# Performance work log

Measured on AMD Instinct MI355X. Metric: run time of the kernel, lower is better.

Reference implementation:

```python
import jax, jax.numpy as jnp
import numpy as np

# dims matching init_kwargs
B, S, D, DH, E, K = 16, 8192, 256, 512, 8, 2


def setup_inputs() -> dict:
    key = jax.random.key(0)
    k0, k1, k2, k3 = jax.random.split(key, 4)
    scale = 0.02
    x = jax.random.normal(k0, (B, S, D), dtype=jnp.float32)
    gate_w = jax.random.normal(k1, (E, D), dtype=jnp.float32) * scale   # Linear(d_model, E, bias=False): weight [E, D]
    w1 = jax.random.normal(k2, (E, DH, D), dtype=jnp.float32) * scale   # fc1 weight per expert [DH, D]
    b1 = jnp.zeros((E, DH), dtype=jnp.float32)
    w2 = jax.random.normal(k3, (E, D, DH), dtype=jnp.float32) * scale   # fc2 weight per expert [D, DH]
    b2 = jnp.zeros((E, D), dtype=jnp.float32)
    return {"x": x, "gate_w": gate_w, "w1": w1, "b1": b1, "w2": w2, "b2": b2}


def reference(x, gate_w, w1, b1, w2, b2):
    b, s, d = x.shape
    e = gate_w.shape[0]
    xf = x.reshape(-1, d)                      # [T, D]
    T = xf.shape[0]

    # --- TopKRouter ---
    logits = xf @ gate_w.T                     # [T, E]
    probs = jax.nn.softmax(logits, axis=-1)
    topk_p, topk_i = jax.lax.top_k(probs, K)   # [T, K]
    topk_w = topk_p / topk_p.sum(axis=-1, keepdims=True)
    # load-balancing aux loss
    sel_mask = jax.nn.one_hot(topk_i, e, dtype=jnp.float32).sum(axis=1)  # [T, E]
    f_i = sel_mask.mean(axis=0)
    p_i = probs.mean(axis=0)
    aux_loss = e * jnp.sum(f_i * p_i)

    # --- dispatch: dense per-token expert weights (0 for unselected) ---
    dense_w = jnp.zeros((T, e), dtype=x.dtype).at[
        jnp.arange(T)[:, None], topk_i
    ].add(topk_w)                              # [T, E]

    # --- experts: loop over small fixed E; weight is zero for unselected tokens,
    # so this computes the same math as the sparse gather/scatter loop ---
    out = jnp.zeros_like(xf)
    for ei in range(e):
        h = jax.nn.silu(xf @ w1[ei].T + b1[ei])     # [T, DH]
        y = h @ w2[ei].T + b2[ei]                   # [T, D]
        out = out + dense_w[:, ei:ei + 1] * y

    return out.reshape(b, s, d), aux_loss
```

## Files before the change

### kernel.cpp

```cpp
#include <hip/hip_runtime.h>

typedef __attribute__((ext_vector_type(8))) short short8;
typedef __attribute__((ext_vector_type(4))) float f32x4;

#define T_TOK  131072
#define DMODEL 256
#define DHID   512
#define NEXP   8


__device__ __forceinline__ unsigned short f2bf(float f) {
  unsigned int u = __float_as_uint(f);
  u = (u + 0x7FFFu + ((u >> 16) & 1u)) >> 16;
  return (unsigned short)u;
}
__device__ __forceinline__ float bf2f(unsigned short u) {
  return __uint_as_float(((unsigned)u) << 16);
}

__device__ __forceinline__ void gload16(const void* g, void* l) {
  __builtin_amdgcn_global_load_lds(
      (const __attribute__((address_space(1))) void*)g,
      (__attribute__((address_space(3))) void*)l, 16, 0, 0);
}

__global__ void k_wconv(const float* __restrict__ w1, const float* __restrict__ w2,
                        unsigned short* __restrict__ P1, unsigned short* __restrict__ P2) {
  int g = blockIdx.x * 256 + threadIdx.x;
  int e = g >> 14, rem = g & 16383;
  {
    int row = rem >> 5, c = rem & 31;
    int kc = c >> 3, cs = c & 7;
    const float* s = w1 + ((size_t)e * DHID + row) * DMODEL + c * 8;
    short8 v;
#pragma unroll
    for (int j = 0; j < 8; ++j) v[j] = (short)f2bf(s[j]);
    size_t dc = ((size_t)(e * 4 + kc) * 512 + row) * 8 + (cs ^ (row & 7));
    *(short8*)(P1 + dc * 8) = v;
  }
  {
    int row = rem >> 6, c = rem & 63;
    int kc = c >> 3, cs = c & 7;
    const float* s = w2 + ((size_t)e * DMODEL + row) * DHID + c * 8;
    short8 v;
#pragma unroll
    for (int j = 0; j < 8; ++j) v[j] = (short)f2bf(s[j]);
    size_t dc = ((size_t)(e * 8 + kc) * 256 + row) * 8 + (cs ^ (row & 7));
    *(short8*)(P2 + dc * 8) = v;
  }
}

__global__ __launch_bounds__(256) void k_router(
    const float* __restrict__ x, const float* __restrict__ gate,
    unsigned short* __restrict__ xb, int* __restrict__ pack, float2* __restrict__ tkw,
    int* __restrict__ part_cnt, float* __restrict__ part_psum) {
  __shared__ float g[NEXP][DMODEL];
  __shared__ int s_cnt[NEXP];
  __shared__ float s_ps[NEXP];
  int tid = threadIdx.x;
  for (int i = tid; i < NEXP * DMODEL; i += 256) g[i >> 8][i & 255] = gate[i];
  if (tid < NEXP) { s_cnt[tid] = 0; s_ps[tid] = 0.f; }
  __syncthreads();
  int lane = tid & 63, wv = tid >> 6;
  float psacc[NEXP] = {0.f,0.f,0.f,0.f,0.f,0.f,0.f,0.f};
  for (int k = 0; k < 16; ++k) {
    int t = (blockIdx.x << 6) + (wv << 4) + k;
    const float* xr = x + (size_t)t * DMODEL;
    float4 x4 = *(const float4*)(xr + 4 * lane);
    ushort4 u4;
    u4.x = f2bf(x4.x); u4.y = f2bf(x4.y); u4.z = f2bf(x4.z); u4.w = f2bf(x4.w);
    *(ushort4*)(xb + (size_t)t * DMODEL + 4 * lane) = u4;
    double l[NEXP];
#pragma unroll
    for (int e = 0; e < NEXP; ++e) {
      const float4 g4 = *(const float4*)&g[e][4 * lane];
      l[e] = (double)x4.x * (double)g4.x + (double)x4.y * (double)g4.y +
             (double)x4.z * (double)g4.z + (double)x4.w * (double)g4.w;
    }
#pragma unroll
    for (int e = 0; e < NEXP; ++e) {
#pragma unroll
      for (int d = 32; d; d >>= 1) l[e] += __shfl_xor(l[e], d);
    }
    int i1 = 0;
#pragma unroll
    for (int e = 1; e < NEXP; ++e) if (l[e] > l[i1]) i1 = e;
    int i2 = (i1 == 0) ? 1 : 0;
#pragma unroll
    for (int e = 0; e < NEXP; ++e) if (e != i1 && l[e] > l[i2]) i2 = e;
    double m = l[0];
#pragma unroll
    for (int e = 1; e < NEXP; ++e) m = (l[e] > m) ? l[e] : m;
    float pe[NEXP]; float s = 0.f;
#pragma unroll
    for (int e = 0; e < NEXP; ++e) { pe[e] = __expf((float)(l[e] - m)); s += pe[e]; }
    float inv = 1.f / s;
    float p1 = pe[i1] * inv, p2 = pe[i2] * inv;
    float wn = 1.f / (p1 + p2);
    if (lane == 0) {
      pack[t] = i1 | (i2 << 8);
      tkw[t] = make_float2(p1 * wn, p2 * wn);
      atomicAdd(&s_cnt[i1], 1); atomicAdd(&s_cnt[i2], 1);
#pragma unroll
      for (int e = 0; e < NEXP; ++e) psacc[e] += pe[e] * inv;
    }
  }
  if (lane == 0) {
#pragma unroll
    for (int e = 0; e < NEXP; ++e) atomicAdd(&s_ps[e], psacc[e]);
  }
  __syncthreads();
  if (tid < NEXP) {
    part_cnt[blockIdx.x * NEXP + tid] = s_cnt[tid];
    part_psum[blockIdx.x * NEXP + tid] = s_ps[tid];
  }
}

__global__ __launch_bounds__(512) void k_scan(
    const int* __restrict__ part_cnt, const float* __restrict__ part_psum,
    int* __restrict__ block_off, int* __restrict__ cnt_total, float* __restrict__ out) {
  __shared__ float s_ps[NEXP];
  __shared__ int s_ct[NEXP];
  int lane = threadIdx.x & 63, wv = threadIdx.x >> 6;
  int base = lane * 32;
  int lsum = 0; float ps = 0.f;
#pragma unroll 8
  for (int j = 0; j < 32; ++j) {
    lsum += part_cnt[(base + j) * NEXP + wv];
    ps += part_psum[(base + j) * NEXP + wv];
  }
  int incl = lsum;
#pragma unroll
  for (int d = 1; d < 64; d <<= 1) { int t = __shfl_up(incl, d); if (lane >= d) incl += t; }
  int run = incl - lsum;
#pragma unroll 8
  for (int j = 0; j < 32; ++j) {
    int v = part_cnt[(base + j) * NEXP + wv];
    block_off[(base + j) * NEXP + wv] = run;
    run += v;
  }
#pragma unroll
  for (int d = 32; d; d >>= 1) ps += __shfl_xor(ps, d);
  int total = __shfl(incl, 63);
  if (lane == 0) { cnt_total[wv] = total; s_ct[wv] = total; s_ps[wv] = ps; }
  __syncthreads();
  if (threadIdx.x == 0) {
    double aux = 0.0; int rb = 0;
    for (int e = 0; e < NEXP; ++e) {
      aux += ((double)s_ct[e] / 131072.0) * ((double)s_ps[e] / 131072.0);
      cnt_total[8 + e] = rb;
      rb += (s_ct[e] + 255) & ~255;
    }
    out[33554432] = (float)(8.0 * aux);
  }
}

__global__ void k_scatter(const int* __restrict__ pack, float2* tkw,
                          const int* __restrict__ block_off, const int* __restrict__ cnt_total,
                          int* __restrict__ tok_list, float* __restrict__ wt_list) {
  __shared__ int s_loc[NEXP];
  int tid = threadIdx.x;
  if (tid < NEXP) s_loc[tid] = 0;
  __syncthreads();
  int t = (blockIdx.x << 6) + tid;
  int p = pack[t];
  float2 wv = tkw[t];
  int e1 = p & 255, e2 = (p >> 8) & 255;
  int o1 = block_off[blockIdx.x * NEXP + e1];
  int p1 = atomicAdd(&s_loc[e1], 1);
  int i1 = cnt_total[8 + e1] + o1 + p1;
  tok_list[i1] = t; wt_list[i1] = wv.x;
  int o2 = block_off[blockIdx.x * NEXP + e2];
  int p2 = atomicAdd(&s_loc[e2], 1);
  int i2 = cnt_total[8 + e2] + o2 + p2;
  tok_list[i2] = t; wt_list[i2] = wv.y;
  tkw[t] = make_float2(__int_as_float(i1), __int_as_float(i2));
}

__global__ __launch_bounds__(512, 2) void k_gemm1(
    const unsigned short* __restrict__ xb, const unsigned short* __restrict__ P1,
    const float* __restrict__ b1, const int* __restrict__ tok_list,
    const int* __restrict__ cnt_total, unsigned short* __restrict__ Hp) {
  __shared__ __align__(16) unsigned short buf[65536];
  __shared__ int s_tok[128];

  int bid = (blockIdx.x & 7) * 514 + (blockIdx.x >> 3);
  int e = -1, loc = 0, cum = 0, cnte = 0;
#pragma unroll
  for (int ee = 0; ee < NEXP; ++ee) {
    int ct = cnt_total[ee];
    int nb = ((ct + 127) >> 7) * 2;
    if (e < 0 && bid < cum + nb) { e = ee; loc = bid - cum; cnte = ct; }
    cum += nb;
  }
  if (e < 0) return;
  int mi = loc >> 1, ni = loc & 1;
  int nv = cnte - (mi << 7); if (nv > 128) nv = 128;
  int hbp = cnt_total[8 + e];

  int tid = threadIdx.x;
  int lane = tid & 63, w = tid >> 6, l15 = lane & 15, lg = lane >> 4;
  int wr = w >> 2, wc = w & 3;

  float b1v[4];
#pragma unroll
  for (int nt = 0; nt < 4; ++nt)
    b1v[nt] = b1[e * DHID + ni * 256 + wc * 64 + nt * 16 + l15];

  if (tid < 128) s_tok[tid] = tok_list[hbp + (mi << 7) + (tid < nv ? tid : nv - 1)];
  __syncthreads();

  int ar0 = tid >> 5;
  int ac = tid & 31;
#pragma unroll
  for (int i = 0; i < 8; ++i) {
    int row = i * 16 + ar0;
    gload16(xb + (size_t)s_tok[row] * DMODEL + (size_t)((ac ^ (row & 7)) << 3),
            &buf[(size_t)(i * 512 + w * 64) * 8]);
  }
  auto stage_b = [&](int kc) {
    const unsigned short* src = P1 + ((size_t)(e * 4 + kc) * 512 + ni * 256) * 64;
    int d = 32768 + (kc & 1) * 16384;
#pragma unroll
    for (int i = 0; i < 4; ++i) {
      int cidx = i * 512 + tid;
      gload16(src + (size_t)cidx * 8, &buf[d + (i * 512 + w * 64) * 8]);
    }
  };
  stage_b(0);
  asm volatile("s_waitcnt vmcnt(0)" ::: "memory");
  __builtin_amdgcn_s_barrier();
  __builtin_amdgcn_sched_barrier(0);

  int aidx[4][2], bidx[4][2];
#pragma unroll
  for (int mt = 0; mt < 4; ++mt) {
    int r = wr * 64 + mt * 16 + l15, r7 = r & 7;
#pragma unroll
    for (int ks = 0; ks < 2; ++ks) aidx[mt][ks] = r * 256 + (((ks * 4 + lg) ^ r7) << 3);
  }
#pragma unroll
  for (int nt = 0; nt < 4; ++nt) {
    int r = wc * 64 + nt * 16 + l15, r7 = r & 7;
#pragma unroll
    for (int ks = 0; ks < 2; ++ks) bidx[nt][ks] = r * 64 + (((ks * 4 + lg) ^ r7) << 3);
  }

  f32x4 acc[4][4];
#pragma unroll
  for (int mt = 0; mt < 4; ++mt)
#pragma unroll
    for (int nt = 0; nt < 4; ++nt) acc[mt][nt] = (f32x4){0.f, 0.f, 0.f, 0.f};

  for (int s = 0; s < 4; ++s) {
    if (s < 3) stage_b(s + 1);
    int abase = s * 64;
    int bbase = 32768 + (s & 1) * 16384;
#pragma unroll
    for (int ks = 0; ks < 2; ++ks) {
      short8 a[4], b[4];
#pragma unroll
      for (int mt = 0; mt < 4; ++mt) a[mt] = *(const short8*)&buf[abase + aidx[mt][ks]];
#pragma unroll
      for (int nt = 0; nt < 4; ++nt) b[nt] = *(const short8*)&buf[bbase + bidx[nt][ks]];
#pragma unroll
      for (int mt = 0; mt < 4; ++mt)
#pragma unroll
        for (int nt = 0; nt < 4; ++nt)
          acc[mt][nt] = __builtin_amdgcn_mfma_f32_16x16x32_bf16(a[mt], b[nt], acc[mt][nt], 0, 0, 0);
    }
    asm volatile("s_waitcnt vmcnt(0)" ::: "memory");
    __builtin_amdgcn_s_barrier();
    __builtin_amdgcn_sched_barrier(0);
  }

#pragma unroll
  for (int mt = 0; mt < 4; ++mt) {
    int rbase0 = (wr * 64 + mt * 16) * 256;
#pragma unroll
    for (int nt = 0; nt < 4; ++nt) {
      int col = wc * 64 + nt * 16 + l15;
      int c3 = col >> 3, c7 = col & 7;
#pragma unroll
      for (int rr = 0; rr < 4; ++rr) {
        int lr = lg * 4 + rr;
        int r7 = lr & 7;
        float z = acc[mt][nt][rr] + b1v[nt];
        float sv = z * __builtin_amdgcn_rcpf(1.f + __expf(-z));
        buf[rbase0 + lr * 256 + ((c3 ^ r7) << 3) + c7] =
            (unsigned short)(__float_as_uint(sv) >> 16);
      }
    }
  }
  __syncthreads();
  int blk = (hbp >> 8) + (mi >> 1);
  int rbase = (mi & 1) * 128;
  {
    int s32 = tid & 31;
    int c32 = s32 ^ (ar0 & 7);
    int kc = ni * 4 + (c32 >> 3), cs = c32 & 7;
    size_t gb = (((size_t)(blk * 8 + kc) * 256 + rbase + ar0) * 8 + (size_t)(cs ^ (ar0 & 7))) * 8;
    int lb = ar0 * 256 + s32 * 8;
    short8 z8 = {0, 0, 0, 0, 0, 0, 0, 0};
#pragma unroll
    for (int i = 0; i < 8; ++i) {
      int row = i * 16 + ar0;
      short8 v = (row < nv) ? *(const short8*)&buf[lb + i * 4096] : z8;
      *(short8*)&Hp[gb + (size_t)i * 1024] = v;
    }
  }
}

__global__ __launch_bounds__(512, 2) void k_gemm2c(
    unsigned short* Hp, const unsigned short* __restrict__ P2,
    const float* __restrict__ b2, const float* __restrict__ wt_list,
    const int* __restrict__ cnt_total) {
  __shared__ __align__(16) unsigned short buf[65536];
  __shared__ float s_wt[256];

  int bid = (blockIdx.x & 7) * 129 + (blockIdx.x >> 3);
  int e = -1, mi = 0, cum = 0, cnte = 0;
#pragma unroll
  for (int ee = 0; ee < NEXP; ++ee) {
    int ct = cnt_total[ee];
    int nb = (ct + 255) >> 8;
    if (e < 0 && bid < cum + nb) { e = ee; mi = bid - cum; cnte = ct; }
    cum += nb;
  }
  if (e < 0) return;
  int nv = cnte - (mi << 8); if (nv > 256) nv = 256;
  int hbp = cnt_total[8 + e];
  int blk = (hbp >> 8) + mi;

  int tid = threadIdx.x;
  int lane = tid & 63, w = tid >> 6, l15 = lane & 15, lg = lane >> 4;
  int wr = w >> 2, wc = w & 3;

  float b2v[4];
#pragma unroll
  for (int nt = 0; nt < 4; ++nt)
    b2v[nt] = b2[e * DMODEL + wc * 64 + nt * 16 + l15];

  if (tid < 256) s_wt[tid] = (tid < nv) ? wt_list[hbp + (mi << 8) + tid] : 0.f;
  __syncthreads();

  auto stage = [&](int s) {
    int d = (s & 1) * 32768;
    const unsigned short* sa = Hp + (size_t)(blk * 8 + s) * 16384;
    const unsigned short* sb = P2 + (size_t)(e * 8 + s) * 16384;
#pragma unroll
    for (int i = 0; i < 4; ++i) {
      int c = i * 512 + tid;
      gload16(sa + (size_t)c * 8, &buf[d + (i * 512 + w * 64) * 8]);
    }
#pragma unroll
    for (int i = 0; i < 4; ++i) {
      int c = i * 512 + tid;
      gload16(sb + (size_t)c * 8, &buf[d + 16384 + (i * 512 + w * 64) * 8]);
    }
  };

  int aidx[8][2], bidx[4][2];
#pragma unroll
  for (int mt = 0; mt < 8; ++mt) {
    int r = wr * 128 + mt * 16 + l15, r7 = r & 7;
#pragma unroll
    for (int ks = 0; ks < 2; ++ks) aidx[mt][ks] = r * 64 + (((ks * 4 + lg) ^ r7) << 3);
  }
#pragma unroll
  for (int nt = 0; nt < 4; ++nt) {
    int r = wc * 64 + nt * 16 + l15, r7 = r & 7;
#pragma unroll
    for (int ks = 0; ks < 2; ++ks) bidx[nt][ks] = r * 64 + (((ks * 4 + lg) ^ r7) << 3);
  }

  f32x4 acc[8][4];
#pragma unroll
  for (int mt = 0; mt < 8; ++mt)
#pragma unroll
    for (int nt = 0; nt < 4; ++nt) acc[mt][nt] = (f32x4){0.f, 0.f, 0.f, 0.f};

  stage(0);
  asm volatile("s_waitcnt vmcnt(0)" ::: "memory");
  __builtin_amdgcn_s_barrier();
  __builtin_amdgcn_sched_barrier(0);

  for (int s = 0; s < 8; ++s) {
    if (s < 7) stage(s + 1);
    int ab = (s & 1) * 32768, bb = ab + 16384;
#pragma unroll
    for (int ks = 0; ks < 2; ++ks) {
      short8 a[8], b[4];
#pragma unroll
      for (int mt = 0; mt < 8; ++mt) a[mt] = *(const short8*)&buf[ab + aidx[mt][ks]];
#pragma unroll
      for (int nt = 0; nt < 4; ++nt) b[nt] = *(const short8*)&buf[bb + bidx[nt][ks]];
#pragma unroll
      for (int mt = 0; mt < 8; ++mt)
#pragma unroll
        for (int nt = 0; nt < 4; ++nt)
          acc[mt][nt] = __builtin_amdgcn_mfma_f32_16x16x32_bf16(a[mt], b[nt], acc[mt][nt], 0, 0, 0);
    }
    asm volatile("s_waitcnt vmcnt(0)" ::: "memory");
    __builtin_amdgcn_s_barrier();
    __builtin_amdgcn_sched_barrier(0);
  }

#pragma unroll
  for (int mt = 0; mt < 8; ++mt) {
    int rbase0 = (wr * 128 + mt * 16) * 256;
#pragma unroll
    for (int nt = 0; nt < 4; ++nt) {
      int col = wc * 64 + nt * 16 + l15;
#pragma unroll
      for (int rr = 0; rr < 4; ++rr) {
        int row = wr * 128 + mt * 16 + lg * 4 + rr;
        float v = s_wt[row] * (acc[mt][nt][rr] + b2v[nt]);
        buf[rbase0 + (lg * 4 + rr) * 256 + col] =
            (unsigned short)(__float_as_uint(v) >> 16);
      }
    }
  }
  __syncthreads();
  unsigned short* ydst = Hp + (size_t)blk * 131072;
#pragma unroll
  for (int i = 0; i < 16; ++i) {
    size_t cidx = (size_t)(i * 512 + tid) * 8;
    *(short8*)&ydst[cidx] = *(const short8*)&buf[cidx];
  }
}

__global__ __launch_bounds__(256) void k_reduce(
    const unsigned short* __restrict__ Y, const float2* __restrict__ inv,
    float* __restrict__ out) {
  int g = blockIdx.x * 256 + threadIdx.x;
#pragma unroll
  for (int it = 0; it < 8; ++it) {
    int t = g >> 5;
    int cw = (g & 31) << 3;
    float2 iv = inv[t];
    int s1 = __float_as_int(iv.x), s2 = __float_as_int(iv.y);
    const unsigned short* y1 = Y + (size_t)(s1 >> 8) * 131072 + (size_t)(s1 & 255) * 256 + cw;
    const unsigned short* y2 = Y + (size_t)(s2 >> 8) * 131072 + (size_t)(s2 & 255) * 256 + cw;
    short8 a = *(const short8*)y1;
    short8 b = *(const short8*)y2;
    float* op = out + (size_t)t * 256 + cw;
    float4 r0, r1;
    r0.x = bf2f((unsigned short)a[0]) + bf2f((unsigned short)b[0]);
    r0.y = bf2f((unsigned short)a[1]) + bf2f((unsigned short)b[1]);
    r0.z = bf2f((unsigned short)a[2]) + bf2f((unsigned short)b[2]);
    r0.w = bf2f((unsigned short)a[3]) + bf2f((unsigned short)b[3]);
    r1.x = bf2f((unsigned short)a[4]) + bf2f((unsigned short)b[4]);
    r1.y = bf2f((unsigned short)a[5]) + bf2f((unsigned short)b[5]);
    r1.z = bf2f((unsigned short)a[6]) + bf2f((unsigned short)b[6]);
    r1.w = bf2f((unsigned short)a[7]) + bf2f((unsigned short)b[7]);
    *(float4*)op = r0;
    *(float4*)(op + 4) = r1;
    g += 2048 * 256;
  }
}

extern "C" void kernel_launch(void* const* d_in, const int* in_sizes, int n_in,
                              void* d_out, int out_size, void* d_ws, size_t ws_size,
                              hipStream_t stream) {
  const float* x    = (const float*)d_in[0];
  const float* gate = (const float*)d_in[1];
  const float* w1   = (const float*)d_in[2];
  const float* b1   = (const float*)d_in[3];
  const float* w2   = (const float*)d_in[4];
  const float* b2   = (const float*)d_in[5];
  float* out = (float*)d_out;
  char* ws = (char*)d_ws;

  unsigned short* xb  = (unsigned short*)(ws);
  unsigned short* P1  = (unsigned short*)(ws + 67108864);
  unsigned short* P2  = (unsigned short*)(ws + 69206016);
  int*    tok_list  = (int*)(ws + 71303168);
  float*  wt_list   = (float*)(ws + 72368128);
  int*    pack      = (int*)(ws + 73433088);
  float2* tkw       = (float2*)(ws + 73957376);
  int*    part_cnt  = (int*)(ws + 75005952);
  float*  part_psum = (float*)(ws + 75071488);
  int*    block_off = (int*)(ws + 75137024);
  int*    cnt_total = (int*)(ws + 75202560);
  unsigned short* Hp = (unsigned short*)(ws + 75497472);

  k_wconv<<<512, 256, 0, stream>>>(w1, w2, P1, P2);
  k_router<<<2048, 256, 0, stream>>>(x, gate, xb, pack, tkw, part_cnt, part_psum);
  k_scan<<<1, 512, 0, stream>>>(part_cnt, part_psum, block_off, cnt_total, out);
  k_scatter<<<2048, 64, 0, stream>>>(pack, tkw, block_off, cnt_total, tok_list, wt_list);
  k_gemm1<<<4112, 512, 0, stream>>>(xb, P1, b1, tok_list, cnt_total, Hp);
  k_gemm2c<<<1032, 512, 0, stream>>>(Hp, P2, b2, wt_list, cnt_total);
  k_reduce<<<2048, 256, 0, stream>>>(Hp, tkw, out);
}
```

Baseline: 546.1 us.

## Restructure router to thread-per-token dot products with LDS-staged x

The router kernel previously used one wavefront per token, with butterfly shuffle reductions over doubles for all 8 experts. It now stages 64 tokens of x in swizzled shared memory and gives each thread one token and a quarter of the model dimension. Partial logits are combined through a shared-memory reduction across the four wavefronts. Gate weights are pre-converted to double in the weight-conversion kernel and read straight from global memory, which removes per-element float-to-double conversion and the shuffle chains. The cost is extra __syncthreads, 64KB+ of LDS per block, and a grid that drops to 512 blocks while keeping the same partial-count layout.

```diff
diff --git a/kernel.cpp b/kernel.cpp
--- a/kernel.cpp
+++ b/kernel.cpp
@@ -25,8 +25,11 @@
 }
 
 __global__ void k_wconv(const float* __restrict__ w1, const float* __restrict__ w2,
-                        unsigned short* __restrict__ P1, unsigned short* __restrict__ P2) {
+                        const float* __restrict__ gate,
+                        unsigned short* __restrict__ P1, unsigned short* __restrict__ P2,
+                        double* __restrict__ gate_d) {
   int g = blockIdx.x * 256 + threadIdx.x;
+  if (g < 2048) gate_d[g] = (double)gate[g];
   int e = g >> 14, rem = g & 16383;
   {
     int row = rem >> 5, c = rem & 31;
@@ -50,69 +53,99 @@
   }
 }
 
-__global__ __launch_bounds__(256) void k_router(
-    const float* __restrict__ x, const float* __restrict__ gate,
+__global__ __launch_bounds__(256, 2) void k_router(
+    const float* __restrict__ x, const double* __restrict__ gd,
     unsigned short* __restrict__ xb, int* __restrict__ pack, float2* __restrict__ tkw,
     int* __restrict__ part_cnt, float* __restrict__ part_psum) {
-  __shared__ float g[NEXP][DMODEL];
+  __shared__ float xs[16384];
+  __shared__ double red[1024];
   __shared__ int s_cnt[NEXP];
   __shared__ float s_ps[NEXP];
   int tid = threadIdx.x;
-  for (int i = tid; i < NEXP * DMODEL; i += 256) g[i >> 8][i & 255] = gate[i];
-  if (tid < NEXP) { s_cnt[tid] = 0; s_ps[tid] = 0.f; }
-  __syncthreads();
-  int lane = tid & 63, wv = tid >> 6;
-  float psacc[NEXP] = {0.f,0.f,0.f,0.f,0.f,0.f,0.f,0.f};
-  for (int k = 0; k < 16; ++k) {
-    int t = (blockIdx.x << 6) + (wv << 4) + k;
-    const float* xr = x + (size_t)t * DMODEL;
-    float4 x4 = *(const float4*)(xr + 4 * lane);
-    ushort4 u4;
-    u4.x = f2bf(x4.x); u4.y = f2bf(x4.y); u4.z = f2bf(x4.z); u4.w = f2bf(x4.w);
-    *(ushort4*)(xb + (size_t)t * DMODEL + 4 * lane) = u4;
-    double l[NEXP];
-#pragma unroll
-    for (int e = 0; e < NEXP; ++e) {
-      const float4 g4 = *(const float4*)&g[e][4 * lane];
-      l[e] = (double)x4.x * (double)g4.x + (double)x4.y * (double)g4.y +
-             (double)x4.z * (double)g4.z + (double)x4.w * (double)g4.w;
-    }
-#pragma unroll
-    for (int e = 0; e < NEXP; ++e) {
-#pragma unroll
-      for (int d = 32; d; d >>= 1) l[e] += __shfl_xor(l[e], d);
-    }
-    int i1 = 0;
-#pragma unroll
-    for (int e = 1; e < NEXP; ++e) if (l[e] > l[i1]) i1 = e;
-    int i2 = (i1 == 0) ? 1 : 0;
-#pragma unroll
-    for (int e = 0; e < NEXP; ++e) if (e != i1 && l[e] > l[i2]) i2 = e;
-    double m = l[0];
-#pragma unroll
-    for (int e = 1; e < NEXP; ++e) m = (l[e] > m) ? l[e] : m;
-    float pe[NEXP]; float s = 0.f;
-#pragma unroll
-    for (int e = 0; e < NEXP; ++e) { pe[e] = __expf((float)(l[e] - m)); s += pe[e]; }
-    float inv = 1.f / s;
-    float p1 = pe[i1] * inv, p2 = pe[i2] * inv;
-    float wn = 1.f / (p1 + p2);
-    if (lane == 0) {
+  int tok = tid & 63, q = tid >> 6;
+  int qu = __builtin_amdgcn_readfirstlane(q);
+
+  for (int c = 0; c < 4; ++c) {
+    if (tid < NEXP) { s_cnt[tid] = 0; s_ps[tid] = 0.f; }
+    int tb = (blockIdx.x << 8) + (c << 6);
+    __syncthreads();
+
+#pragma unroll
+    for (int i = 0; i < 16; ++i) {
+      int idx = i * 256 + tid;
+      int row = idx >> 6, c4 = (idx & 63) << 2;
+      float4 v = *(const float4*)(x + (size_t)(tb + row) * 256 + c4);
+      int sw = row & 31;
+      float* xr = xs + row * 256;
+      xr[(c4 + 0) ^ sw] = v.x;
+      xr[(c4 + 1) ^ sw] = v.y;
+      xr[(c4 + 2) ^ sw] = v.z;
+      xr[(c4 + 3) ^ sw] = v.w;
+      ushort4 u4;
+      u4.x = f2bf(v.x); u4.y = f2bf(v.y); u4.z = f2bf(v.z); u4.w = f2bf(v.w);
+      *(ushort4*)(xb + (size_t)(tb + row) * 256 + c4) = u4;
+    }
+    __syncthreads();
+
+    double acc[8] = {0, 0, 0, 0, 0, 0, 0, 0};
+    {
+      int sw = tok & 31;
+      const float* xr = xs + tok * 256;
+#pragma unroll 4
+      for (int d0 = 0; d0 < 64; ++d0) {
+        int d = (qu << 6) + d0;
+        double xv = (double)xr[d ^ sw];
+#pragma unroll
+        for (int e = 0; e < 8; ++e) acc[e] += xv * gd[e * 256 + d];
+      }
+    }
+
+    double l[8];
+#pragma unroll
+    for (int j = 0; j < 4; ++j) red[tid * 4 + j] = acc[j];
+    __syncthreads();
+    if (tid < 64) {
+#pragma unroll
+      for (int j = 0; j < 4; ++j)
+        l[j] = red[tid * 4 + j] + red[(64 + tid) * 4 + j] +
+               red[(128 + tid) * 4 + j] + red[(192 + tid) * 4 + j];
+    }
+    __syncthreads();
+#pragma unroll
+    for (int j = 0; j < 4; ++j) red[tid * 4 + j] = acc[4 + j];
+    __syncthreads();
+    if (tid < 64) {
+#pragma unroll
+      for (int j = 0; j < 4; ++j)
+        l[4 + j] = red[tid * 4 + j] + red[(64 + tid) * 4 + j] +
+                   red[(128 + tid) * 4 + j] + red[(192 + tid) * 4 + j];
+      int t = tb + tid;
+      int i1 = 0;
+#pragma unroll
+      for (int e = 1; e < NEXP; ++e) if (l[e] > l[i1]) i1 = e;
+      int i2 = (i1 == 0) ? 1 : 0;
+#pragma unroll
+      for (int e = 0; e < NEXP; ++e) if (e != i1 && l[e] > l[i2]) i2 = e;
+      double m = l[0];
+#pragma unroll
+      for (int e = 1; e < NEXP; ++e) m = (l[e] > m) ? l[e] : m;
+      float pe[NEXP]; float s = 0.f;
+#pragma unroll
+      for (int e = 0; e < NEXP; ++e) { pe[e] = __expf((float)(l[e] - m)); s += pe[e]; }
+      float inv = 1.f / s;
+      float p1 = pe[i1] * inv, p2 = pe[i2] * inv;
+      float wn = 1.f / (p1 + p2);
       pack[t] = i1 | (i2 << 8);
       tkw[t] = make_float2(p1 * wn, p2 * wn);
       atomicAdd(&s_cnt[i1], 1); atomicAdd(&s_cnt[i2], 1);
 #pragma unroll
-      for (int e = 0; e < NEXP; ++e) psacc[e] += pe[e] * inv;
-    }
-  }
-  if (lane == 0) {
-#pragma unroll
-    for (int e = 0; e < NEXP; ++e) atomicAdd(&s_ps[e], psacc[e]);
-  }
-  __syncthreads();
-  if (tid < NEXP) {
-    part_cnt[blockIdx.x * NEXP + tid] = s_cnt[tid];
-    part_psum[blockIdx.x * NEXP + tid] = s_ps[tid];
+      for (int e = 0; e < NEXP; ++e) atomicAdd(&s_ps[e], pe[e] * inv);
+    }
+    __syncthreads();
+    if (tid < NEXP) {
+      part_cnt[(blockIdx.x * 4 + c) * NEXP + tid] = s_cnt[tid];
+      part_psum[(blockIdx.x * 4 + c) * NEXP + tid] = s_ps[tid];
+    }
   }
 }
 
@@ -483,10 +516,11 @@
   float*  part_psum = (float*)(ws + 75071488);
   int*    block_off = (int*)(ws + 75137024);
   int*    cnt_total = (int*)(ws + 75202560);
+  double* gate_d    = (double*)(ws + 75235328);
   unsigned short* Hp = (unsigned short*)(ws + 75497472);
 
-  k_wconv<<<512, 256, 0, stream>>>(w1, w2, P1, P2);
-  k_router<<<2048, 256, 0, stream>>>(x, gate, xb, pack, tkw, part_cnt, part_psum);
+  k_wconv<<<512, 256, 0, stream>>>(w1, w2, gate, P1, P2, gate_d);
+  k_router<<<512, 256, 0, stream>>>(x, gate_d, xb, pack, tkw, part_cnt, part_psum);
   k_scan<<<1, 512, 0, stream>>>(part_cnt, part_psum, block_off, cnt_total, out);
   k_scatter<<<2048, 64, 0, stream>>>(pack, tkw, block_off, cnt_total, tok_list, wt_list);
   k_gemm1<<<4112, 512, 0, stream>>>(xb, P1, b1, tok_list, cnt_total, Hp);
```

Measured after the change: 503.6 us. -7.8%, faster.
